# Optimization experiments

Measured on AMD Instinct MI355X. Metric: run time of the kernel, lower is better.

The kernel has to match this reference:

```python
import jax, jax.numpy as jnp
import numpy as np

B, L, D = 8, 128, 768
H = 300              # lstm hidden per direction
WMAX = 5             # max span window
NZ = int(L * 0.5)    # span_pruned_threshold = 0.5
SPAN_W_DIM, DIST_DIM, FF = 20, 128, 150
TARGET_DIM, REL_DIM = 3, 4
SPAN_DIM = 2 * 2 * H + SPAN_W_DIM           # 1220
PAIR_DIM = 2 * SPAN_DIM + DIST_DIM          # 2568


def _span_indices(length, wmax):
    starts, ends = [], []
    for w in range(1, wmax + 1):
        s = np.arange(0, length - w + 1)
        starts.append(s)
        ends.append(s + w - 1)
    return np.concatenate(starts), np.concatenate(ends)

_STARTS_NP, _ENDS_NP = _span_indices(L, WMAX)   # Ns = 5L - 10 = 630
_STARTS = jnp.asarray(_STARTS_NP, jnp.int32)
_ENDS = jnp.asarray(_ENDS_NP, jnp.int32)
_WIDTHS = _ENDS - _STARTS + 1                   # width embedding index = j - i + 1


def setup_inputs() -> dict:
    key = jax.random.key(0)
    ks = jax.random.split(key, 16)
    g = lambda i, shape, s=0.05: jax.random.normal(ks[i], shape, dtype=jnp.float32) * s
    z = lambda *shape: jnp.zeros(shape, jnp.float32)
    return {
        'x': jax.random.normal(ks[0], (B, L, D), dtype=jnp.float32),
        'Wih_f': g(1, (4 * H, D)), 'Whh_f': g(2, (4 * H, H)), 'bih_f': z(4 * H), 'bhh_f': z(4 * H),
        'Wih_b': g(3, (4 * H, D)), 'Whh_b': g(4, (4 * H, H)), 'bih_b': z(4 * H), 'bhh_b': z(4 * H),
        'width_emb': g(5, (512, SPAN_W_DIM), 1.0),
        'dist_emb': g(6, (512, DIST_DIM), 1.0),
        'sw1': g(7, (FF, SPAN_DIM)), 'sb1': z(FF),
        'sw2': g(8, (FF, FF)), 'sb2': z(FF),
        'sw3': g(9, (TARGET_DIM, FF)), 'sb3': z(TARGET_DIM),
        'pw1': g(10, (FF, PAIR_DIM)), 'pb1': z(FF),
        'pw2': g(11, (FF, FF)), 'pb2': z(FF),
        'pw3': g(12, (REL_DIM, FF)), 'pb3': z(REL_DIM),
    }


def _lstm_dir(x_tbd, Wih, Whh, bih, bhh):
    """x_tbd: [L, B, D] -> hidden states [L, B, H] (PyTorch LSTM gate order i,f,g,o)."""
    nb = x_tbd.shape[1]
    xg = jnp.einsum('lbd,gd->lbg', x_tbd, Wih) + bih + bhh  # precompute input projections

    def step(carry, xt):
        h, c = carry
        gates = xt + h @ Whh.T
        i, f, gg, o = jnp.split(gates, 4, axis=-1)
        c = jax.nn.sigmoid(f) * c + jax.nn.sigmoid(i) * jnp.tanh(gg)
        h = jax.nn.sigmoid(o) * jnp.tanh(c)
        return (h, c), h

    init = (jnp.zeros((nb, H), x_tbd.dtype), jnp.zeros((nb, H), x_tbd.dtype))
    _, hs = jax.lax.scan(step, init, xg)
    return hs


def _ffnn(zz, w1, b1, w2, b2, w3, b3):
    zz = jax.nn.relu(zz @ w1.T + b1)
    zz = jax.nn.relu(zz @ w2.T + b2)
    return jax.nn.softmax(zz @ w3.T + b3, axis=-1)


def _forward(x, Wih_f, Whh_f, bih_f, bhh_f, Wih_b, Whh_b, bih_b, bhh_b,
             width_emb, dist_emb, sw1, sb1, sw2, sb2, sw3, sb3,
             pw1, pb1, pw2, pb2, pw3, pb3):
    nb = x.shape[0]
    xt = jnp.swapaxes(x, 0, 1)                                  # [L, B, D]
    hf = _lstm_dir(xt, Wih_f, Whh_f, bih_f, bhh_f)
    hb = _lstm_dir(xt[::-1], Wih_b, Whh_b, bih_b, bhh_b)[::-1]
    out = jnp.swapaxes(jnp.concatenate([hf, hb], -1), 0, 1)     # [B, L, 600]

    # span representation: [h_i ; h_j ; width_emb(j-i+1)] -> [B, Ns, 1220]
    wfeat = jnp.broadcast_to(width_emb[_WIDTHS][None], (nb, _STARTS.shape[0], SPAN_W_DIM))
    spans = jnp.concatenate([out[:, _STARTS_NP], out[:, _ENDS_NP], wfeat], axis=-1)

    spans_probability = _ffnn(spans, sw1, sb1, sw2, sb2, sw3, sb3)  # [B, Ns, 3]

    # topk pruning: ASPECT=1, OPINION=2
    t_idx = jax.lax.top_k(spans_probability[:, :, 1], NZ)[1]    # [B, NZ]
    o_idx = jax.lax.top_k(spans_probability[:, :, 2], NZ)[1]

    # itertools.product order: target varies slowest
    pair_t = jnp.repeat(t_idx, NZ, axis=1)                       # [B, NZ*NZ]
    pair_o = jnp.tile(o_idx, (1, NZ))

    a, b = _STARTS[pair_t], _ENDS[pair_t]
    c, d = _STARTS[pair_o], _ENDS[pair_o]
    dist = jnp.minimum(jnp.abs(b - c), jnp.abs(a - d))           # min(|b-c|, |a-d|)

    t_span = jnp.take_along_axis(spans, pair_t[:, :, None], axis=1)
    o_span = jnp.take_along_axis(spans, pair_o[:, :, None], axis=1)
    candidates = jnp.concatenate([t_span, o_span, dist_emb[dist]], axis=-1)  # [B, NZ^2, 2568]

    candidate_probability = _ffnn(candidates, pw1, pb1, pw2, pb2, pw3, pb3)  # [B, NZ^2, 4]
    return spans_probability, candidate_probability, t_idx, o_idx


def reference(x, Wih_f, Whh_f, bih_f, bhh_f, Wih_b, Whh_b, bih_b, bhh_b,
              width_emb, dist_emb, sw1, sb1, sw2, sb2, sw3, sb3,
              pw1, pb1, pw2, pb2, pw3, pb3):
    sp, cp, t_idx, o_idx = _forward(x, Wih_f, Whh_f, bih_f, bhh_f, Wih_b, Whh_b, bih_b, bhh_b,
                                    width_emb, dist_emb, sw1, sb1, sw2, sb2, sw3, sb3,
                                    pw1, pb1, pw2, pb2, pw3, pb3)
    return (sp, cp, t_idx, o_idx)
```

## Files before the change

### kernel.cpp

```cpp
#include <hip/hip_runtime.h>
#include <stdint.h>
#include <stddef.h>

#define BB   8
#define LL   128
#define DD   768
#define HH   300
#define G4   1200
#define NSP  630
#define FFD  150
#define NZK  64

#define WPD  60
#define JC   5

__device__ __forceinline__ float sigm(float x){ return 1.0f/(1.0f+expf(-x)); }

__device__ __forceinline__ void span_decode(int s, int& w, int& i){
  if      (s < 128){ w=1; i=s; }
  else if (s < 255){ w=2; i=s-128; }
  else if (s < 381){ w=3; i=s-255; }
  else if (s < 506){ w=4; i=s-381; }
  else             { w=5; i=s-506; }
}

__device__ __forceinline__ uint64_t shfl_xor_u64(uint64_t v, int m){
  uint32_t lo = (uint32_t)v, hi = (uint32_t)(v >> 32);
  lo = (uint32_t)__shfl_xor((int)lo, m, 64);
  hi = (uint32_t)__shfl_xor((int)hi, m, 64);
  return ((uint64_t)hi << 32) | lo;
}

__global__ __launch_bounds__(256) void k_xg(
    const float* __restrict__ x,
    const float* __restrict__ WihF, const float* __restrict__ bihF, const float* __restrict__ bhhF,
    const float* __restrict__ WihB, const float* __restrict__ bihB, const float* __restrict__ bhhB,
    float* __restrict__ xg, int* __restrict__ tags)
{
  if (blockIdx.x==0 && blockIdx.y==0 && blockIdx.z==0) {
    for (int i = threadIdx.x; i < 2*60*32; i += 256)
      __hip_atomic_store(&tags[i], 0, __ATOMIC_RELAXED, __HIP_MEMORY_SCOPE_AGENT);
  }
  const int dir = blockIdx.z;
  const float* Wih = dir ? WihB : WihF;
  const float* bi  = dir ? bihB : bihF;
  const float* bh  = dir ? bhhB : bhhF;
  const int r0 = blockIdx.x * 64;
  const int n0 = blockIdx.y * 64;
  __shared__ __align__(16) float As[16*68];
  __shared__ __align__(16) float Bs[16*68];
  const int tid = threadIdx.x;
  const int rl = tid >> 2, kq = tid & 3;
  const int tx = tid & 15, ty = tid >> 4;
  float acc[4][4] = {};
  for (int k0 = 0; k0 < DD; k0 += 16) {
    float4 a4 = make_float4(0.f,0.f,0.f,0.f);
    int ra = r0 + rl;
    if (ra < G4) a4 = *(const float4*)&Wih[ra*DD + k0 + kq*4];
    As[(kq*4+0)*68 + rl] = a4.x;
    As[(kq*4+1)*68 + rl] = a4.y;
    As[(kq*4+2)*68 + rl] = a4.z;
    As[(kq*4+3)*68 + rl] = a4.w;
    int n = n0 + rl; int tt = n >> 3, bb = n & 7;
    float4 b4 = *(const float4*)&x[(bb*LL + tt)*DD + k0 + kq*4];
    Bs[(kq*4+0)*68 + rl] = b4.x;
    Bs[(kq*4+1)*68 + rl] = b4.y;
    Bs[(kq*4+2)*68 + rl] = b4.z;
    Bs[(kq*4+3)*68 + rl] = b4.w;
    __syncthreads();
    #pragma unroll
    for (int kk = 0; kk < 16; ++kk) {
      float4 av = *(const float4*)&As[kk*68 + tx*4];
      float4 bv = *(const float4*)&Bs[kk*68 + ty*4];
      float a_[4] = {av.x,av.y,av.z,av.w};
      float b_[4] = {bv.x,bv.y,bv.z,bv.w};
      #pragma unroll
      for (int i=0;i<4;i++)
        #pragma unroll
        for (int j=0;j<4;j++)
          acc[i][j] = fmaf(a_[i], b_[j], acc[i][j]);
    }
    __syncthreads();
  }
  #pragma unroll
  for (int i=0;i<4;i++){
    int r = r0 + tx*4 + i;
    if (r >= G4) continue;
    float bias = bi[r] + bh[r];
    #pragma unroll
    for (int j=0;j<4;j++){
      int n = n0 + ty*4 + j; int tt = n>>3, bb = n&7;
      xg[((dir*LL + tt)*G4 + r)*8 + bb] = acc[i][j] + bias;
    }
  }
}

__global__ __launch_bounds__(320) void k_lstm(
    const float* __restrict__ WhhF, const float* __restrict__ WhhB,
    const float* __restrict__ xg,
    float* __restrict__ hexf,
    int* __restrict__ tags,
    float* __restrict__ out)
{
  const int wg  = blockIdx.x;
  const int dir = wg / WPD;
  const int wid = wg - dir*WPD;
  const int j0  = wid * JC;
  const float* Whh = dir ? WhhB : WhhF;
  float* hex0 = hexf + (size_t)dir*2432;
  int* tg = tags + dir*60*32;

  __shared__ __align__(16) float hls[8*304 + 16];
  __shared__ int hready;

  const int tid  = threadIdx.x;
  const int wv   = tid >> 6;
  const int lane = tid & 63;
  const int rl   = lane >> 4;
  const int s    = lane & 15;
  const int Rabs = rl*HH + j0 + wv;
  const int bb   = s & 7;

  float4 w4[5];
  #pragma unroll
  for (int q=0;q<5;q++){
    int k = s*20 + q*4;
    if (k + 3 < HH) w4[q] = *(const float4*)&Whh[(size_t)Rabs*HH + k];
    else            w4[q] = make_float4(0.f,0.f,0.f,0.f);
  }
  float creg = 0.f;
  if (tid == 0) hready = 0;
  {
    float4* h4 = (float4*)hls;
    for (int i = tid; i < 612; i += 320) h4[i] = make_float4(0.f,0.f,0.f,0.f);
  }
  __syncthreads();

  float xg_c = xg[((size_t)(dir*LL + (dir ? LL-1 : 0))*G4 + Rabs)*8 + bb];

  for (int t = 0; t < LL; ++t) {
    const int tOrig = dir ? (LL-1 - t) : t;
    float xg_n = 0.f;
    if (t+1 < LL) {
      int tO2 = dir ? (LL-2 - t) : (t+1);
      xg_n = xg[((size_t)(dir*LL + tO2)*G4 + Rabs)*8 + bb];
    }
    if (t > 0) {
      if (wv == 0) {
        if (lane < 60) {
          while (__hip_atomic_load(&tg[lane*32], __ATOMIC_RELAXED,
                                   __HIP_MEMORY_SCOPE_AGENT) < t)
            __builtin_amdgcn_s_sleep(1);
        }
        if (lane == 0) ((volatile int*)&hready)[0] = t;
      } else {
        while (((volatile int*)&hready)[0] < t) __builtin_amdgcn_s_sleep(1);
      }
      if (tid < 304) {
        const float* p0 = hex0 + (size_t)(t&1)*4864 + tid*8;
        float4 v0, v1;
        asm volatile(
          "global_load_dwordx4 %0, %2, off sc0 sc1\n\t"
          "global_load_dwordx4 %1, %3, off sc0 sc1\n\t"
          "s_waitcnt vmcnt(0)"
          : "=v"(v0), "=v"(v1)
          : "v"(p0), "v"(p0 + 4)
          : "memory");
        float4* d = (float4*)&hls[tid*8];
        d[0] = v0; d[1] = v1;
      }
    }
    __syncthreads();
    float p[8];
    {
      const float4* h4 = (const float4*)hls;
      #pragma unroll
      for (int b=0;b<8;b++){
        const float4* hb = h4 + b*76 + s*5;
        float ax=0.f, ay=0.f, az=0.f, aw=0.f;
        #pragma unroll
        for (int q=0;q<5;q++){
          float4 hv = hb[q];
          ax = fmaf(w4[q].x, hv.x, ax);
          ay = fmaf(w4[q].y, hv.y, ay);
          az = fmaf(w4[q].z, hv.z, az);
          aw = fmaf(w4[q].w, hv.w, aw);
        }
        p[b] = (ax+ay)+(az+aw);
      }
    }
    #pragma unroll
    for (int b=0;b<8;b++) p[b] += __shfl_xor(p[b], 8, 64);
    float q4[4];
    #pragma unroll
    for (int b=0;b<4;b++){
      float mine = (s&4) ? p[b+4] : p[b];
      float oth  = (s&4) ? p[b]   : p[b+4];
      q4[b] = mine + __shfl_xor(oth, 4, 64);
    }
    float q2[2];
    #pragma unroll
    for (int b=0;b<2;b++){
      float mine = (s&2) ? q4[b+2] : q4[b];
      float oth  = (s&2) ? q4[b]   : q4[b+2];
      q2[b] = mine + __shfl_xor(oth, 2, 64);
    }
    float gv;
    {
      float mine = (s&1) ? q2[1] : q2[0];
      float oth  = (s&1) ? q2[0] : q2[1];
      gv = mine + __shfl_xor(oth, 1, 64) + xg_c;
    }
    {
      int bsel = lane & 7;
      float g_i = __shfl(gv,      bsel, 64);
      float g_f = __shfl(gv, 16 + bsel, 64);
      float g_g = __shfl(gv, 32 + bsel, 64);
      float g_o = __shfl(gv, 48 + bsel, 64);
      if (lane < 8) {
        int b = lane;
        float ig = sigm(g_i), fg = sigm(g_f), gg = tanhf(g_g), og = sigm(g_o);
        creg = fg * creg + ig * gg;
        float h = og * tanhf(creg);
        out[((size_t)(b*LL + tOrig))*600 + dir*HH + j0 + wv] = h;
        if (t+1 < LL)
          __hip_atomic_store(&hex0[(size_t)((t+1)&1)*4864 + b*304 + j0 + wv], h,
                             __ATOMIC_RELAXED, __HIP_MEMORY_SCOPE_AGENT);
      }
    }
    __syncthreads();
    if (t+1 < LL && tid == 0)
      __hip_atomic_store(&tg[wid*32], t+1,
                         __ATOMIC_RELAXED, __HIP_MEMORY_SCOPE_AGENT);
    xg_c = xg_n;
  }
}

__global__ __launch_bounds__(320) void k_uv(
    const float* __restrict__ out, const float* __restrict__ sw1, float* __restrict__ UV)
{
  const int half = blockIdx.z;
  const int row0 = blockIdx.x * 32;
  __shared__ float As[16*36];
  __shared__ __align__(16) float Wt[16*172];
  const int tid = threadIdx.x;
  const int pg = tid / 20, ng = tid - (tid/20)*20;
  float acc[2][8] = {};
  for (int k0 = 0; k0 < 600; k0 += 16) {
    for (int idx = tid; idx < 512; idx += 320) {
      int p = idx >> 4, kk = idx & 15;
      int k = k0 + kk;
      As[kk*36 + p] = (k < 600) ? out[(row0 + p)*600 + k] : 0.f;
    }
    for (int idx = tid; idx < 16*160; idx += 320) {
      int n = idx >> 4, kk = idx & 15;
      int k = k0 + kk;
      Wt[kk*172 + n] = (n < FFD && k < 600) ? sw1[n*1220 + half*600 + k] : 0.f;
    }
    __syncthreads();
    #pragma unroll
    for (int kk=0;kk<16;kk++){
      float2 a2 = *(const float2*)&As[kk*36 + pg*2];
      float4 w0 = *(const float4*)&Wt[kk*172 + ng*8];
      float4 w1 = *(const float4*)&Wt[kk*172 + ng*8 + 4];
      float a_[2] = {a2.x, a2.y};
      float w_[8] = {w0.x,w0.y,w0.z,w0.w,w1.x,w1.y,w1.z,w1.w};
      #pragma unroll
      for (int i=0;i<2;i++)
        #pragma unroll
        for (int j=0;j<8;j++)
          acc[i][j] = fmaf(a_[i], w_[j], acc[i][j]);
    }
    __syncthreads();
  }
  #pragma unroll
  for (int i=0;i<2;i++){
    int row = row0 + pg*2 + i;
    #pragma unroll
    for (int j=0;j<8;j++){
      int n = ng*8 + j;
      if (n < FFD) UV[row*300 + half*FFD + n] = acc[i][j];
    }
  }
}

__global__ __launch_bounds__(160) void k_const(
    const float* __restrict__ sw1, const float* __restrict__ wemb, float* __restrict__ wcst,
    const float* __restrict__ pw1, const float* __restrict__ demb, float* __restrict__ Zd)
{
  int n = threadIdx.x;
  if (n >= FFD) return;
  if (blockIdx.x < 6) {
    int w = blockIdx.x;
    float a = 0.f;
    for (int k=0;k<20;k++) a = fmaf(sw1[n*1220 + 1200 + k], wemb[w*20 + k], a);
    wcst[w*FFD + n] = a;
  } else {
    int d = blockIdx.x - 6;
    float a = 0.f;
    for (int k=0;k<128;k++) a = fmaf(pw1[n*2568 + 2440 + k], demb[d*128 + k], a);
    Zd[d*FFD + n] = a;
  }
}

__global__ __launch_bounds__(320) void k_spanhead(
    const float* __restrict__ UV, const float* __restrict__ wcst,
    const float* __restrict__ sb1,
    const float* __restrict__ sw2, const float* __restrict__ sb2,
    const float* __restrict__ sw3, const float* __restrict__ sb3,
    float* __restrict__ sp)
{
  const int b  = blockIdx.y;
  const int s0 = blockIdx.x * 64;
  __shared__ __align__(16) float z1T[160*68];
  __shared__ __align__(16) float z2T[160*68];
  __shared__ __align__(16) float Wt[16*172];
  __shared__ float zf[256];
  __shared__ int sI[64], sJ[64], sW[64];
  const int tid = threadIdx.x;
  if (tid < 64) {
    int s = s0 + tid; int w = 1, i0 = 0;
    if (s < NSP) span_decode(s, w, i0);
    sI[tid] = i0; sJ[tid] = i0 + w - 1; sW[tid] = w;
  }
  __syncthreads();
  for (int idx = tid; idx < 64*160; idx += 320) {
    int p = idx / 160, k = idx - p*160;
    float v = 0.f;
    if (k < FFD && (s0 + p) < NSP) {
      v = UV[(b*LL + sI[p])*300 + k] + UV[(b*LL + sJ[p])*300 + FFD + k]
        + wcst[sW[p]*FFD + k] + sb1[k];
      v = fmaxf(v, 0.f);
    }
    z1T[k*68 + p] = v;
  }
  const int pg = tid / 20, ng = tid - (tid/20)*20;
  float acc[4][8] = {};
  for (int kt = 0; kt < 10; ++kt) {
    __syncthreads();
    for (int idx = tid; idx < 16*160; idx += 320) {
      int n = idx >> 4, kk = idx & 15;
      int k = kt*16 + kk;
      Wt[kk*172 + n] = (n < FFD && k < FFD) ? sw2[n*FFD + k] : 0.f;
    }
    __syncthreads();
    #pragma unroll
    for (int kk = 0; kk < 16; ++kk) {
      float4 a4 = *(const float4*)&z1T[(kt*16+kk)*68 + pg*4];
      float4 w0 = *(const float4*)&Wt[kk*172 + ng*8];
      float4 w1 = *(const float4*)&Wt[kk*172 + ng*8 + 4];
      float a_[4] = {a4.x,a4.y,a4.z,a4.w};
      float w_[8] = {w0.x,w0.y,w0.z,w0.w,w1.x,w1.y,w1.z,w1.w};
      #pragma unroll
      for (int i=0;i<4;i++)
        #pragma unroll
        for (int j=0;j<8;j++)
          acc[i][j] = fmaf(a_[i], w_[j], acc[i][j]);
    }
  }
  __syncthreads();
  #pragma unroll
  for (int j=0;j<8;j++){
    int n = ng*8 + j;
    float bn = (n < FFD) ? sb2[n] : 0.f;
    #pragma unroll
    for (int i=0;i<4;i++){
      float v = (n < FFD) ? fmaxf(acc[i][j] + bn, 0.f) : 0.f;
      z2T[n*68 + pg*4 + i] = v;
    }
  }
  __syncthreads();
  if (tid < 256) {
    int p = tid >> 2, c = tid & 3;
    if (c < 3 && (s0 + p) < NSP) {
      float a = sb3[c];
      for (int k=0;k<FFD;k++) a = fmaf(z2T[k*68 + p], sw3[c*FFD + k], a);
      zf[p*4 + c] = a;
    }
  }
  __syncthreads();
  if (tid < 64 && (s0 + tid) < NSP) {
    float z0 = zf[tid*4], z1 = zf[tid*4+1], z2 = zf[tid*4+2];
    float m = fmaxf(z0, fmaxf(z1, z2));
    float e0 = expf(z0-m), e1 = expf(z1-m), e2 = expf(z2-m);
    float inv = 1.f/(e0+e1+e2);
    int s = s0 + tid;
    sp[(b*NSP + s)*3 + 0] = e0*inv;
    sp[(b*NSP + s)*3 + 1] = e1*inv;
    sp[(b*NSP + s)*3 + 2] = e2*inv;
  }
}

__global__ __launch_bounds__(64) void k_topk(
    const float* __restrict__ sp, float* __restrict__ outT, float* __restrict__ outO,
    int* __restrict__ idxw)
{
  const int cls = blockIdx.x >> 3;
  const int b   = blockIdx.x & 7;
  const int lane = threadIdx.x;
  uint64_t key[10];
  #pragma unroll
  for (int q=0;q<10;q++){
    int s = lane + q*64;
    uint32_t bits = 0u;
    if (s < NSP) bits = __float_as_uint(sp[(b*NSP + s)*3 + 1 + cls]);
    key[q] = ((uint64_t)bits << 32) | (uint32_t)(1023 - s);
  }
  float* dst = cls ? outO : outT;
  for (int r = 0; r < NZK; ++r) {
    uint64_t best = key[0];
    #pragma unroll
    for (int q=1;q<10;q++) best = key[q] > best ? key[q] : best;
    #pragma unroll
    for (int off = 32; off > 0; off >>= 1) {
      uint64_t o = shfl_xor_u64(best, off);
      best = o > best ? o : best;
    }
    int sWin = 1023 - (int)(best & 0xFFFFFFFFu);
    if ((sWin & 63) == lane) {
      int qw = sWin >> 6;
      #pragma unroll
      for (int q=0;q<10;q++) if (q == qw) key[q] = 0;
    }
    if (lane == 0) {
      dst[b*NZK + r] = (float)sWin;
      idxw[cls*512 + b*NZK + r] = sWin;
    }
  }
}

__global__ __launch_bounds__(320) void k_zto(
    const float* __restrict__ out, const float* __restrict__ wemb,
    const float* __restrict__ pw1, const int* __restrict__ idxw,
    float* __restrict__ ZTO)
{
  const int wg = blockIdx.x;
  const int cls = wg >> 5;
  const int rem = wg & 31;
  const int b = rem >> 2;
  const int i0 = (rem & 3) * 16;
  __shared__ float As[16*20];
  __shared__ __align__(16) float Wt[16*172];
  __shared__ int sI[16], sJ[16], sW[16];
  const int tid = threadIdx.x;
  if (tid < 16) {
    int S = idxw[cls*512 + b*64 + i0 + tid];
    int w, i_; span_decode(S, w, i_);
    sI[tid] = i_; sJ[tid] = i_ + w - 1; sW[tid] = w;
  }
  const int pg = tid / 20, ng = tid - (tid/20)*20;
  float acc[8] = {};
  __syncthreads();
  for (int k0 = 0; k0 < 1232; k0 += 16) {
    if (tid < 256) {
      int p = tid >> 4, kk = tid & 15;
      int k = k0 + kk;
      float v = 0.f;
      if      (k < 600)  v = out[(b*LL + sI[p])*600 + k];
      else if (k < 1200) v = out[(b*LL + sJ[p])*600 + (k - 600)];
      else if (k < 1220) v = wemb[sW[p]*20 + (k - 1200)];
      As[kk*20 + p] = v;
    }
    for (int idx = tid; idx < 16*160; idx += 320) {
      int n = idx >> 4, kk = idx & 15;
      int k = k0 + kk;
      Wt[kk*172 + n] = (n < FFD && k < 1220) ? pw1[n*2568 + cls*1220 + k] : 0.f;
    }
    __syncthreads();
    #pragma unroll
    for (int kk=0;kk<16;kk++){
      float a = As[kk*20 + pg];
      float4 w0 = *(const float4*)&Wt[kk*172 + ng*8];
      float4 w1 = *(const float4*)&Wt[kk*172 + ng*8 + 4];
      acc[0] = fmaf(a, w0.x, acc[0]);
      acc[1] = fmaf(a, w0.y, acc[1]);
      acc[2] = fmaf(a, w0.z, acc[2]);
      acc[3] = fmaf(a, w0.w, acc[3]);
      acc[4] = fmaf(a, w1.x, acc[4]);
      acc[5] = fmaf(a, w1.y, acc[5]);
      acc[6] = fmaf(a, w1.z, acc[6]);
      acc[7] = fmaf(a, w1.w, acc[7]);
    }
    __syncthreads();
  }
  #pragma unroll
  for (int j=0;j<8;j++){
    int n = ng*8 + j;
    if (n < FFD) ZTO[(cls*512 + b*64 + i0 + pg)*FFD + n] = acc[j];
  }
}

__global__ __launch_bounds__(320) void k_pairhead(
    const float* __restrict__ ZTO, const float* __restrict__ Zd,
    const float* __restrict__ pb1,
    const float* __restrict__ pw2, const float* __restrict__ pb2,
    const float* __restrict__ pw3, const float* __restrict__ pb3,
    const int* __restrict__ idxw,
    float* __restrict__ cp)
{
  const int b  = blockIdx.y;
  const int ti = blockIdx.x;
  __shared__ __align__(16) float z1T[160*68];
  __shared__ __align__(16) float z2T[160*68];
  __shared__ __align__(16) float Wt[16*172];
  __shared__ float zf[256];
  __shared__ int oDist[64];
  const int tid = threadIdx.x;
  const int tS = idxw[b*64 + ti];
  int wT, iT; span_decode(tS, wT, iT);
  const int aT = iT, bT = iT + wT - 1;
  if (tid < 64) {
    int oS = idxw[512 + b*64 + tid];
    int wO, iO; span_decode(oS, wO, iO);
    int d1 = bT - iO;            if (d1 < 0) d1 = -d1;
    int d2 = aT - (iO + wO - 1); if (d2 < 0) d2 = -d2;
    oDist[tid] = d1 < d2 ? d1 : d2;
  }
  __syncthreads();
  const float* ZtRow = ZTO + (b*64 + ti)*FFD;
  for (int idx = tid; idx < 64*160; idx += 320) {
    int p = idx / 160, k = idx - p*160;
    float v = 0.f;
    if (k < FFD) {
      v = ZtRow[k] + ZTO[(512 + b*64 + p)*FFD + k] + Zd[oDist[p]*FFD + k] + pb1[k];
      v = fmaxf(v, 0.f);
    }
    z1T[k*68 + p] = v;
  }
  const int pg = tid / 20, ng = tid - (tid/20)*20;
  float acc[4][8] = {};
  for (int kt = 0; kt < 10; ++kt) {
    __syncthreads();
    for (int idx = tid; idx < 16*160; idx += 320) {
      int n = idx >> 4, kk = idx & 15;
      int k = kt*16 + kk;
      Wt[kk*172 + n] = (n < FFD && k < FFD) ? pw2[n*FFD + k] : 0.f;
    }
    __syncthreads();
    #pragma unroll
    for (int kk = 0; kk < 16; ++kk) {
      float4 a4 = *(const float4*)&z1T[(kt*16+kk)*68 + pg*4];
      float4 w0 = *(const float4*)&Wt[kk*172 + ng*8];
      float4 w1 = *(const float4*)&Wt[kk*172 + ng*8 + 4];
      float a_[4] = {a4.x,a4.y,a4.z,a4.w};
      float w_[8] = {w0.x,w0.y,w0.z,w0.w,w1.x,w1.y,w1.z,w1.w};
      #pragma unroll
      for (int i=0;i<4;i++)
        #pragma unroll
        for (int j=0;j<8;j++)
          acc[i][j] = fmaf(a_[i], w_[j], acc[i][j]);
    }
  }
  __syncthreads();
  #pragma unroll
  for (int j=0;j<8;j++){
    int n = ng*8 + j;
    float bn = (n < FFD) ? pb2[n] : 0.f;
    #pragma unroll
    for (int i=0;i<4;i++){
      float v = (n < FFD) ? fmaxf(acc[i][j] + bn, 0.f) : 0.f;
      z2T[n*68 + pg*4 + i] = v;
    }
  }
  __syncthreads();
  if (tid < 256) {
    int p = tid >> 2, c = tid & 3;
    float a = pb3[c];
    for (int k=0;k<FFD;k++) a = fmaf(z2T[k*68 + p], pw3[c*FFD + k], a);
    zf[tid] = a;
  }
  __syncthreads();
  if (tid < 64) {
    float z0 = zf[tid*4], z1 = zf[tid*4+1], z2 = zf[tid*4+2], z3 = zf[tid*4+3];
    float m = fmaxf(fmaxf(z0,z1), fmaxf(z2,z3));
    float e0 = expf(z0-m), e1 = expf(z1-m), e2 = expf(z2-m), e3 = expf(z3-m);
    float inv = 1.f/(e0+e1+e2+e3);
    float4 o4 = make_float4(e0*inv, e1*inv, e2*inv, e3*inv);
    *(float4*)&cp[(size_t)((b*4096 + ti*64 + tid))*4] = o4;
  }
}

extern "C" void kernel_launch(void* const* d_in, const int* in_sizes, int n_in,
                              void* d_out, int out_size, void* d_ws, size_t ws_size,
                              hipStream_t stream) {
  const float* x    = (const float*)d_in[0];
  const float* WihF = (const float*)d_in[1];
  const float* WhhF = (const float*)d_in[2];
  const float* bihF = (const float*)d_in[3];
  const float* bhhF = (const float*)d_in[4];
  const float* WihB = (const float*)d_in[5];
  const float* WhhB = (const float*)d_in[6];
  const float* bihB = (const float*)d_in[7];
  const float* bhhB = (const float*)d_in[8];
  const float* wemb = (const float*)d_in[9];
  const float* demb = (const float*)d_in[10];
  const float* sw1  = (const float*)d_in[11];
  const float* sb1  = (const float*)d_in[12];
  const float* sw2  = (const float*)d_in[13];
  const float* sb2  = (const float*)d_in[14];
  const float* sw3  = (const float*)d_in[15];
  const float* sb3  = (const float*)d_in[16];
  const float* pw1  = (const float*)d_in[17];
  const float* pb1  = (const float*)d_in[18];
  const float* pw2  = (const float*)d_in[19];
  const float* pb2  = (const float*)d_in[20];
  const float* pw3  = (const float*)d_in[21];
  const float* pb3  = (const float*)d_in[22];

  uint8_t* wsb = (uint8_t*)d_ws;
  int*   tags  = (int*)wsb;
  float* hexf  = (float*)(wsb + 16384);
  float* xg    = (float*)(wsb + 131072);
  float* outh  = xg   + 2457600;
  float* UV    = outh + 614400;
  float* wcst  = UV   + 307200;
  float* Zd    = wcst + 900;
  float* ZTO   = Zd   + 38400;
  int*  idxw   = (int*)(ZTO + 153600);

  float* o   = (float*)d_out;
  float* spO = o;
  float* cpO = o + 15120;
  float* tO  = o + 146192;
  float* oO  = o + 146704;

  k_xg      <<<dim3(19,16,2), 256, 0, stream>>>(x, WihF, bihF, bhhF, WihB, bihB, bhhB, xg, tags);
  k_lstm    <<<dim3(2*WPD), 320, 0, stream>>>(WhhF, WhhB, xg, hexf, tags, outh);
  k_uv      <<<dim3(32,1,2), 320, 0, stream>>>(outh, sw1, UV);
  k_const   <<<dim3(262), 160, 0, stream>>>(sw1, wemb, wcst, pw1, demb, Zd);
  k_spanhead<<<dim3(10,8), 320, 0, stream>>>(UV, wcst, sb1, sw2, sb2, sw3, sb3, spO);
  k_topk    <<<dim3(16),  64, 0, stream>>>(spO, tO, oO, idxw);
  k_zto     <<<dim3(64),  320, 0, stream>>>(outh, wemb, pw1, idxw, ZTO);
  k_pairhead<<<dim3(64,8), 320, 0, stream>>>(ZTO, Zd, pb1, pw2, pb2, pw3, pb3, idxw, cpO);
}
```

Measured before the change: 1.210 ms.

## Fold constant tables into xg kernel, split LSTM launch, widen grids of head kernels

Constant projection tables (width and distance embeddings times first-layer weights) are now computed by an extra z-slice of the input-projection kernel, which removes one launch. The LSTM recurrence is split into two launches of 64 steps, with the cell state stashed between them. The UV, span-head and ZTO kernels use smaller row tiles or a split-K scheme, so their grids have more blocks. The pair head sums the two split-K partial ZTO buffers. The LSTM split adds a launch and relaunch cost and reloads the weights, and the smaller tiles reduce reuse per block.

```diff
diff --git a/kernel.cpp b/kernel.cpp
--- a/kernel.cpp
+++ b/kernel.cpp
@@ -35,8 +35,27 @@
     const float* __restrict__ x,
     const float* __restrict__ WihF, const float* __restrict__ bihF, const float* __restrict__ bhhF,
     const float* __restrict__ WihB, const float* __restrict__ bihB, const float* __restrict__ bhhB,
-    float* __restrict__ xg, int* __restrict__ tags)
+    float* __restrict__ xg, int* __restrict__ tags,
+    const float* __restrict__ sw1, const float* __restrict__ wemb, float* __restrict__ wcst,
+    const float* __restrict__ pw1, const float* __restrict__ demb, float* __restrict__ Zd)
 {
+  if (blockIdx.z == 2) {
+    int cb = blockIdx.y*19 + blockIdx.x;
+    int n = threadIdx.x;
+    if (n < FFD) {
+      if (cb < 6) {
+        float a = 0.f;
+        for (int k=0;k<20;k++) a = fmaf(sw1[n*1220 + 1200 + k], wemb[cb*20 + k], a);
+        wcst[cb*FFD + n] = a;
+      } else if (cb < 262) {
+        int d = cb - 6;
+        float a = 0.f;
+        for (int k=0;k<128;k++) a = fmaf(pw1[n*2568 + 2440 + k], demb[d*128 + k], a);
+        Zd[d*FFD + n] = a;
+      }
+    }
+    return;
+  }
   if (blockIdx.x==0 && blockIdx.y==0 && blockIdx.z==0) {
     for (int i = threadIdx.x; i < 2*60*32; i += 256)
       __hip_atomic_store(&tags[i], 0, __ATOMIC_RELAXED, __HIP_MEMORY_SCOPE_AGENT);
@@ -100,7 +119,9 @@
     const float* __restrict__ xg,
     float* __restrict__ hexf,
     int* __restrict__ tags,
-    float* __restrict__ out)
+    float* __restrict__ out,
+    float* __restrict__ cstash,
+    int t0, int t1)
 {
   const int wg  = blockIdx.x;
   const int dir = wg / WPD;
@@ -118,7 +139,8 @@
   const int lane = tid & 63;
   const int rl   = lane >> 4;
   const int s    = lane & 15;
-  const int Rabs = rl*HH + j0 + wv;
+  const int jj   = j0 + wv;
+  const int Rabs = rl*HH + jj;
   const int bb   = s & 7;
 
   float4 w4[5];
@@ -129,6 +151,8 @@
     else            w4[q] = make_float4(0.f,0.f,0.f,0.f);
   }
   float creg = 0.f;
+  if (t0 > 0 && lane < 8)
+    creg = cstash[((size_t)wg*JC + wv)*8 + lane];
   if (tid == 0) hready = 0;
   {
     float4* h4 = (float4*)hls;
@@ -136,12 +160,12 @@
   }
   __syncthreads();
 
-  float xg_c = xg[((size_t)(dir*LL + (dir ? LL-1 : 0))*G4 + Rabs)*8 + bb];
-
-  for (int t = 0; t < LL; ++t) {
+  float xg_c = xg[((size_t)(dir*LL + (dir ? LL-1 - t0 : t0))*G4 + Rabs)*8 + bb];
+
+  for (int t = t0; t < t1; ++t) {
     const int tOrig = dir ? (LL-1 - t) : t;
     float xg_n = 0.f;
-    if (t+1 < LL) {
+    if (t+1 < t1) {
       int tO2 = dir ? (LL-2 - t) : (t+1);
       xg_n = xg[((size_t)(dir*LL + tO2)*G4 + Rabs)*8 + bb];
     }
@@ -222,9 +246,9 @@
         float ig = sigm(g_i), fg = sigm(g_f), gg = tanhf(g_g), og = sigm(g_o);
         creg = fg * creg + ig * gg;
         float h = og * tanhf(creg);
-        out[((size_t)(b*LL + tOrig))*600 + dir*HH + j0 + wv] = h;
+        out[((size_t)(b*LL + tOrig))*600 + dir*HH + jj] = h;
         if (t+1 < LL)
-          __hip_atomic_store(&hex0[(size_t)((t+1)&1)*4864 + b*304 + j0 + wv], h,
+          __hip_atomic_store(&hex0[(size_t)(((t+1)&1))*4864 + b*304 + jj], h,
                              __ATOMIC_RELAXED, __HIP_MEMORY_SCOPE_AGENT);
       }
     }
@@ -234,23 +258,25 @@
                          __ATOMIC_RELAXED, __HIP_MEMORY_SCOPE_AGENT);
     xg_c = xg_n;
   }
+  if (t1 < LL && lane < 8)
+    cstash[((size_t)wg*JC + wv)*8 + lane] = creg;
 }
 
 __global__ __launch_bounds__(320) void k_uv(
     const float* __restrict__ out, const float* __restrict__ sw1, float* __restrict__ UV)
 {
   const int half = blockIdx.z;
-  const int row0 = blockIdx.x * 32;
-  __shared__ float As[16*36];
+  const int row0 = blockIdx.x * 16;
+  __shared__ float As[16*20];
   __shared__ __align__(16) float Wt[16*172];
   const int tid = threadIdx.x;
   const int pg = tid / 20, ng = tid - (tid/20)*20;
-  float acc[2][8] = {};
+  float acc[8] = {};
   for (int k0 = 0; k0 < 600; k0 += 16) {
-    for (int idx = tid; idx < 512; idx += 320) {
-      int p = idx >> 4, kk = idx & 15;
+    if (tid < 256) {
+      int p = tid >> 4, kk = tid & 15;
       int k = k0 + kk;
-      As[kk*36 + p] = (k < 600) ? out[(row0 + p)*600 + k] : 0.f;
+      As[kk*20 + p] = (k < 600) ? out[(row0 + p)*600 + k] : 0.f;
     }
     for (int idx = tid; idx < 16*160; idx += 320) {
       int n = idx >> 4, kk = idx & 15;
@@ -260,7 +286,74 @@
     __syncthreads();
     #pragma unroll
     for (int kk=0;kk<16;kk++){
-      float2 a2 = *(const float2*)&As[kk*36 + pg*2];
+      float a = As[kk*20 + pg];
+      float4 w0 = *(const float4*)&Wt[kk*172 + ng*8];
+      float4 w1 = *(const float4*)&Wt[kk*172 + ng*8 + 4];
+      acc[0] = fmaf(a, w0.x, acc[0]);
+      acc[1] = fmaf(a, w0.y, acc[1]);
+      acc[2] = fmaf(a, w0.z, acc[2]);
+      acc[3] = fmaf(a, w0.w, acc[3]);
+      acc[4] = fmaf(a, w1.x, acc[4]);
+      acc[5] = fmaf(a, w1.y, acc[5]);
+      acc[6] = fmaf(a, w1.z, acc[6]);
+      acc[7] = fmaf(a, w1.w, acc[7]);
+    }
+    __syncthreads();
+  }
+  {
+    int row = row0 + pg;
+    #pragma unroll
+    for (int j=0;j<8;j++){
+      int n = ng*8 + j;
+      if (n < FFD) UV[row*300 + half*FFD + n] = acc[j];
+    }
+  }
+}
+
+__global__ __launch_bounds__(320) void k_spanhead(
+    const float* __restrict__ UV, const float* __restrict__ wcst,
+    const float* __restrict__ sb1,
+    const float* __restrict__ sw2, const float* __restrict__ sb2,
+    const float* __restrict__ sw3, const float* __restrict__ sb3,
+    float* __restrict__ sp)
+{
+  const int b  = blockIdx.y;
+  const int s0 = blockIdx.x * 32;
+  __shared__ __align__(16) float z1T[160*36];
+  __shared__ __align__(16) float z2T[160*36];
+  __shared__ __align__(16) float Wt[16*172];
+  __shared__ float zf[128];
+  __shared__ int sI[32], sJ[32], sW[32];
+  const int tid = threadIdx.x;
+  if (tid < 32) {
+    int s = s0 + tid; int w = 1, i0 = 0;
+    if (s < NSP) span_decode(s, w, i0);
+    sI[tid] = i0; sJ[tid] = i0 + w - 1; sW[tid] = w;
+  }
+  __syncthreads();
+  for (int idx = tid; idx < 32*160; idx += 320) {
+    int p = idx / 160, k = idx - p*160;
+    float v = 0.f;
+    if (k < FFD && (s0 + p) < NSP) {
+      v = UV[(b*LL + sI[p])*300 + k] + UV[(b*LL + sJ[p])*300 + FFD + k]
+        + wcst[sW[p]*FFD + k] + sb1[k];
+      v = fmaxf(v, 0.f);
+    }
+    z1T[k*36 + p] = v;
+  }
+  const int pg = tid / 20, ng = tid - (tid/20)*20;
+  float acc[2][8] = {};
+  for (int kt = 0; kt < 10; ++kt) {
+    __syncthreads();
+    for (int idx = tid; idx < 16*160; idx += 320) {
+      int n = idx >> 4, kk = idx & 15;
+      int k = kt*16 + kk;
+      Wt[kk*172 + n] = (n < FFD && k < FFD) ? sw2[n*FFD + k] : 0.f;
+    }
+    __syncthreads();
+    #pragma unroll
+    for (int kk = 0; kk < 16; ++kk) {
+      float2 a2 = *(const float2*)&z1T[(kt*16+kk)*36 + pg*2];
       float4 w0 = *(const float4*)&Wt[kk*172 + ng*8];
       float4 w1 = *(const float4*)&Wt[kk*172 + ng*8 + 4];
       float a_[2] = {a2.x, a2.y};
@@ -271,92 +364,6 @@
         for (int j=0;j<8;j++)
           acc[i][j] = fmaf(a_[i], w_[j], acc[i][j]);
     }
-    __syncthreads();
-  }
-  #pragma unroll
-  for (int i=0;i<2;i++){
-    int row = row0 + pg*2 + i;
-    #pragma unroll
-    for (int j=0;j<8;j++){
-      int n = ng*8 + j;
-      if (n < FFD) UV[row*300 + half*FFD + n] = acc[i][j];
-    }
-  }
-}
-
-__global__ __launch_bounds__(160) void k_const(
-    const float* __restrict__ sw1, const float* __restrict__ wemb, float* __restrict__ wcst,
-    const float* __restrict__ pw1, const float* __restrict__ demb, float* __restrict__ Zd)
-{
-  int n = threadIdx.x;
-  if (n >= FFD) return;
-  if (blockIdx.x < 6) {
-    int w = blockIdx.x;
-    float a = 0.f;
-    for (int k=0;k<20;k++) a = fmaf(sw1[n*1220 + 1200 + k], wemb[w*20 + k], a);
-    wcst[w*FFD + n] = a;
-  } else {
-    int d = blockIdx.x - 6;
-    float a = 0.f;
-    for (int k=0;k<128;k++) a = fmaf(pw1[n*2568 + 2440 + k], demb[d*128 + k], a);
-    Zd[d*FFD + n] = a;
-  }
-}
-
-__global__ __launch_bounds__(320) void k_spanhead(
-    const float* __restrict__ UV, const float* __restrict__ wcst,
-    const float* __restrict__ sb1,
-    const float* __restrict__ sw2, const float* __restrict__ sb2,
-    const float* __restrict__ sw3, const float* __restrict__ sb3,
-    float* __restrict__ sp)
-{
-  const int b  = blockIdx.y;
-  const int s0 = blockIdx.x * 64;
-  __shared__ __align__(16) float z1T[160*68];
-  __shared__ __align__(16) float z2T[160*68];
-  __shared__ __align__(16) float Wt[16*172];
-  __shared__ float zf[256];
-  __shared__ int sI[64], sJ[64], sW[64];
-  const int tid = threadIdx.x;
-  if (tid < 64) {
-    int s = s0 + tid; int w = 1, i0 = 0;
-    if (s < NSP) span_decode(s, w, i0);
-    sI[tid] = i0; sJ[tid] = i0 + w - 1; sW[tid] = w;
-  }
-  __syncthreads();
-  for (int idx = tid; idx < 64*160; idx += 320) {
-    int p = idx / 160, k = idx - p*160;
-    float v = 0.f;
-    if (k < FFD && (s0 + p) < NSP) {
-      v = UV[(b*LL + sI[p])*300 + k] + UV[(b*LL + sJ[p])*300 + FFD + k]
-        + wcst[sW[p]*FFD + k] + sb1[k];
-      v = fmaxf(v, 0.f);
-    }
-    z1T[k*68 + p] = v;
-  }
-  const int pg = tid / 20, ng = tid - (tid/20)*20;
-  float acc[4][8] = {};
-  for (int kt = 0; kt < 10; ++kt) {
-    __syncthreads();
-    for (int idx = tid; idx < 16*160; idx += 320) {
-      int n = idx >> 4, kk = idx & 15;
-      int k = kt*16 + kk;
-      Wt[kk*172 + n] = (n < FFD && k < FFD) ? sw2[n*FFD + k] : 0.f;
-    }
-    __syncthreads();
-    #pragma unroll
-    for (int kk = 0; kk < 16; ++kk) {
-      float4 a4 = *(const float4*)&z1T[(kt*16+kk)*68 + pg*4];
-      float4 w0 = *(const float4*)&Wt[kk*172 + ng*8];
-      float4 w1 = *(const float4*)&Wt[kk*172 + ng*8 + 4];
-      float a_[4] = {a4.x,a4.y,a4.z,a4.w};
-      float w_[8] = {w0.x,w0.y,w0.z,w0.w,w1.x,w1.y,w1.z,w1.w};
-      #pragma unroll
-      for (int i=0;i<4;i++)
-        #pragma unroll
-        for (int j=0;j<8;j++)
-          acc[i][j] = fmaf(a_[i], w_[j], acc[i][j]);
-    }
   }
   __syncthreads();
   #pragma unroll
@@ -364,22 +371,22 @@
     int n = ng*8 + j;
     float bn = (n < FFD) ? sb2[n] : 0.f;
     #pragma unroll
-    for (int i=0;i<4;i++){
+    for (int i=0;i<2;i++){
       float v = (n < FFD) ? fmaxf(acc[i][j] + bn, 0.f) : 0.f;
-      z2T[n*68 + pg*4 + i] = v;
-    }
-  }
-  __syncthreads();
-  if (tid < 256) {
+      z2T[n*36 + pg*2 + i] = v;
+    }
+  }
+  __syncthreads();
+  if (tid < 128) {
     int p = tid >> 2, c = tid & 3;
     if (c < 3 && (s0 + p) < NSP) {
       float a = sb3[c];
-      for (int k=0;k<FFD;k++) a = fmaf(z2T[k*68 + p], sw3[c*FFD + k], a);
+      for (int k=0;k<FFD;k++) a = fmaf(z2T[k*36 + p], sw3[c*FFD + k], a);
       zf[p*4 + c] = a;
     }
   }
   __syncthreads();
-  if (tid < 64 && (s0 + tid) < NSP) {
+  if (tid < 32 && (s0 + tid) < NSP) {
     float z0 = zf[tid*4], z1 = zf[tid*4+1], z2 = zf[tid*4+2];
     float m = fmaxf(z0, fmaxf(z1, z2));
     float e0 = expf(z0-m), e1 = expf(z1-m), e2 = expf(z2-m);
@@ -434,11 +441,14 @@
     const float* __restrict__ pw1, const int* __restrict__ idxw,
     float* __restrict__ ZTO)
 {
-  const int wg = blockIdx.x;
-  const int cls = wg >> 5;
-  const int rem = wg & 31;
+  const int kh  = blockIdx.x >> 6;
+  const int r6  = blockIdx.x & 63;
+  const int cls = r6 >> 5;
+  const int rem = r6 & 31;
   const int b = rem >> 2;
   const int i0 = (rem & 3) * 16;
+  const int kbeg = kh ? 640 : 0;
+  const int kend = kh ? 1232 : 640;
   __shared__ float As[16*20];
   __shared__ __align__(16) float Wt[16*172];
   __shared__ int sI[16], sJ[16], sW[16];
@@ -451,7 +461,7 @@
   const int pg = tid / 20, ng = tid - (tid/20)*20;
   float acc[8] = {};
   __syncthreads();
-  for (int k0 = 0; k0 < 1232; k0 += 16) {
+  for (int k0 = kbeg; k0 < kend; k0 += 16) {
     if (tid < 256) {
       int p = tid >> 4, kk = tid & 15;
       int k = k0 + kk;
@@ -486,7 +496,7 @@
   #pragma unroll
   for (int j=0;j<8;j++){
     int n = ng*8 + j;
-    if (n < FFD) ZTO[(cls*512 + b*64 + i0 + pg)*FFD + n] = acc[j];
+    if (n < FFD) ZTO[(size_t)kh*153600 + (cls*512 + b*64 + i0 + pg)*FFD + n] = acc[j];
   }
 }
 
@@ -517,12 +527,14 @@
     oDist[tid] = d1 < d2 ? d1 : d2;
   }
   __syncthreads();
-  const float* ZtRow = ZTO + (b*64 + ti)*FFD;
+  const float* Zt0 = ZTO + (b*64 + ti)*FFD;
+  const float* Zt1 = Zt0 + 153600;
   for (int idx = tid; idx < 64*160; idx += 320) {
     int p = idx / 160, k = idx - p*160;
     float v = 0.f;
     if (k < FFD) {
-      v = ZtRow[k] + ZTO[(512 + b*64 + p)*FFD + k] + Zd[oDist[p]*FFD + k] + pb1[k];
+      int os = (512 + b*64 + p)*FFD + k;
+      v = Zt0[k] + Zt1[k] + ZTO[os] + ZTO[153600 + os] + Zd[oDist[p]*FFD + k] + pb1[k];
       v = fmaxf(v, 0.f);
     }
     z1T[k*68 + p] = v;
@@ -610,13 +622,14 @@
   uint8_t* wsb = (uint8_t*)d_ws;
   int*   tags  = (int*)wsb;
   float* hexf  = (float*)(wsb + 16384);
+  float* cstash= (float*)(wsb + 57344);
   float* xg    = (float*)(wsb + 131072);
   float* outh  = xg   + 2457600;
   float* UV    = outh + 614400;
   float* wcst  = UV   + 307200;
   float* Zd    = wcst + 900;
   float* ZTO   = Zd   + 38400;
-  int*  idxw   = (int*)(ZTO + 153600);
+  int*  idxw   = (int*)(ZTO + 307200);
 
   float* o   = (float*)d_out;
   float* spO = o;
@@ -624,12 +637,13 @@
   float* tO  = o + 146192;
   float* oO  = o + 146704;
 
-  k_xg      <<<dim3(19,16,2), 256, 0, stream>>>(x, WihF, bihF, bhhF, WihB, bihB, bhhB, xg, tags);
-  k_lstm    <<<dim3(2*WPD), 320, 0, stream>>>(WhhF, WhhB, xg, hexf, tags, outh);
-  k_uv      <<<dim3(32,1,2), 320, 0, stream>>>(outh, sw1, UV);
-  k_const   <<<dim3(262), 160, 0, stream>>>(sw1, wemb, wcst, pw1, demb, Zd);
-  k_spanhead<<<dim3(10,8), 320, 0, stream>>>(UV, wcst, sb1, sw2, sb2, sw3, sb3, spO);
+  k_xg      <<<dim3(19,16,3), 256, 0, stream>>>(x, WihF, bihF, bhhF, WihB, bihB, bhhB, xg, tags,
+                                                sw1, wemb, wcst, pw1, demb, Zd);
+  k_lstm    <<<dim3(2*WPD), 320, 0, stream>>>(WhhF, WhhB, xg, hexf, tags, outh, cstash, 0, 64);
+  k_lstm    <<<dim3(2*WPD), 320, 0, stream>>>(WhhF, WhhB, xg, hexf, tags, outh, cstash, 64, 128);
+  k_uv      <<<dim3(64,1,2), 320, 0, stream>>>(outh, sw1, UV);
+  k_spanhead<<<dim3(20,8), 320, 0, stream>>>(UV, wcst, sb1, sw2, sb2, sw3, sb3, spO);
   k_topk    <<<dim3(16),  64, 0, stream>>>(spO, tO, oO, idxw);
-  k_zto     <<<dim3(64),  320, 0, stream>>>(outh, wemb, pw1, idxw, ZTO);
+  k_zto     <<<dim3(128), 320, 0, stream>>>(outh, wemb, pw1, idxw, ZTO);
   k_pairhead<<<dim3(64,8), 320, 0, stream>>>(ZTO, Zd, pb1, pw2, pb2, pw3, pb3, idxw, cpO);
 }
```

After: 1.098 ms. 1.1x faster.
